# Optimization experiments

Measured on AMD Instinct MI355X. Metric: run time of the kernel, lower is better.

Reference implementation:

```python
import jax, jax.numpy as jnp
import numpy as np

DEPTH, DIM, HEADS, MLP, P, IMG, C = 6, 512, 8, 2048, 16, 224, 3
NPATCH = (IMG // P) ** 2  # 196
EPS = 1e-5


def setup_inputs() -> dict:
    key = jax.random.key(0)
    ks = jax.random.split(key, 16)
    s = 0.02
    return {
        "img": jax.random.normal(ks[0], (64, C, IMG, IMG), jnp.float32),
        "patch_w": jax.random.normal(ks[1], (DIM, C * P * P), jnp.float32) * s,
        "patch_b": jax.random.normal(ks[2], (DIM,), jnp.float32) * s,
        "cls_token": jax.random.normal(ks[3], (1, 1, DIM), jnp.float32),
        "pos_emb": jax.random.normal(ks[4], (1, NPATCH + 1, DIM), jnp.float32),
        "in_proj_w": jax.random.normal(ks[5], (DEPTH, 3 * DIM, DIM), jnp.float32) * s,
        "in_proj_b": jax.random.normal(ks[6], (DEPTH, 3 * DIM), jnp.float32) * s,
        "out_proj_w": jax.random.normal(ks[7], (DEPTH, DIM, DIM), jnp.float32) * s,
        "out_proj_b": jax.random.normal(ks[8], (DEPTH, DIM), jnp.float32) * s,
        "ln1_w": jnp.ones((DEPTH, DIM), jnp.float32),
        "ln1_b": jnp.zeros((DEPTH, DIM), jnp.float32),
        "fc1_w": jax.random.normal(ks[9], (DEPTH, MLP, DIM), jnp.float32) * s,
        "fc1_b": jax.random.normal(ks[10], (DEPTH, MLP), jnp.float32) * s,
        "fc2_w": jax.random.normal(ks[11], (DEPTH, DIM, MLP), jnp.float32) * s,
        "fc2_b": jax.random.normal(ks[12], (DEPTH, DIM), jnp.float32) * s,
        "ln2_w": jnp.ones((DEPTH, DIM), jnp.float32),
        "ln2_b": jnp.zeros((DEPTH, DIM), jnp.float32),
    }


def _ln(x, w, b):
    m = jnp.mean(x, -1, keepdims=True)
    v = jnp.mean(jnp.square(x - m), -1, keepdims=True)
    return (x - m) * jax.lax.rsqrt(v + EPS) * w + b


def _patchify(img):
    # b c (h p1) (w p2) -> b (h w) (p1 p2 c), lucidrains ViT ordering
    B = img.shape[0]
    g = IMG // P
    x = img.reshape(B, C, g, P, g, P)
    x = x.transpose(0, 2, 4, 3, 5, 1)  # B, h, w, p1, p2, c
    return x.reshape(B, g * g, P * P * C)


def _vit(img, patch_w, patch_b, cls_token, pos_emb, in_proj_w, in_proj_b,
         out_proj_w, out_proj_b, ln1_w, ln1_b, fc1_w, fc1_b, fc2_w, fc2_b,
         ln2_w, ln2_b):
    B = img.shape[0]
    hd = DIM // HEADS
    x = _patchify(img) @ patch_w.T + patch_b          # [B, 196, 512]
    cls = jnp.broadcast_to(cls_token, (B, 1, DIM))
    x = jnp.concatenate([cls, x], axis=1) + pos_emb   # [B, 197, 512]
    N = x.shape[1]
    for i in range(DEPTH):
        res = x
        qkv = x @ in_proj_w[i].T + in_proj_b[i]       # [B, N, 3*512]
        q, k, v = jnp.split(qkv, 3, axis=-1)
        q = q.reshape(B, N, HEADS, hd).transpose(0, 2, 1, 3)
        k = k.reshape(B, N, HEADS, hd).transpose(0, 2, 1, 3)
        v = v.reshape(B, N, HEADS, hd).transpose(0, 2, 1, 3)
        scores = jnp.einsum('bhnd,bhmd->bhnm', q, k) / jnp.sqrt(jnp.float32(hd))
        probs = jax.nn.softmax(scores, axis=-1)
        ctx = jnp.einsum('bhnm,bhmd->bhnd', probs, v)
        ctx = ctx.transpose(0, 2, 1, 3).reshape(B, N, DIM)
        x = ctx @ out_proj_w[i].T + out_proj_b[i] + res
        x = _ln(x, ln1_w[i], ln1_b[i])
        res = x
        h = jax.nn.gelu(x @ fc1_w[i].T + fc1_b[i], approximate=False)
        x = h @ fc2_w[i].T + fc2_b[i] + res
        x = _ln(x, ln2_w[i], ln2_b[i])
    return x[:, 0]  # ToCLS_Slice: forward returns CLS token [B, 512]


def reference(img, patch_w, patch_b, cls_token, pos_emb, in_proj_w, in_proj_b,
              out_proj_w, out_proj_b, ln1_w, ln1_b, fc1_w, fc1_b, fc2_w, fc2_b,
              ln2_w, ln2_b):
    return _vit(img, patch_w, patch_b, cls_token, pos_emb, in_proj_w, in_proj_b,
                out_proj_w, out_proj_b, ln1_w, ln1_b, fc1_w, fc1_b, fc2_w, fc2_b,
                ln2_w, ln2_b)
```

## Files before the change

### kernel.cpp

```cpp
#include <hip/hip_runtime.h>
#include <hip/hip_bf16.h>

typedef __hip_bfloat16 hb;
typedef __bf16 bf16x8 __attribute__((ext_vector_type(8)));
typedef float f32x4 __attribute__((ext_vector_type(4)));

#define N_DEPTH 6
#define N_DIM   512
#define N_HEADS 8
#define N_MLP   2048
#define N_TOK   197
#define N_PATCH 196
#define N_BATCH 64
#define ROWS    (N_BATCH * N_TOK)
#define ROWS_PAD 12672
#define PROWS   (N_BATCH * N_PATCH)

#define OFF_WPATCH 0u
#define OFF_WQKV   786432u
#define OFF_WOUT   10223616u
#define OFF_WFC1   13369344u
#define OFF_WFC2   25952256u
#define OFF_XBF    38535168u
#define OFF_CTX    51511296u
#define OFF_BIG    64487424u
#define OFF_XF     116391936u
#define OFF_H1     142344192u

__device__ __forceinline__ void gl2lds(const hb* g, hb* l) {
    __builtin_amdgcn_global_load_lds((const __attribute__((address_space(1))) unsigned int*)g,
                                     (__attribute__((address_space(3))) unsigned int*)l, 16, 0, 0);
}


__global__ void cvt_bf16_kernel(const float* __restrict__ in, hb* __restrict__ out, int n) {
    int t = blockIdx.x * 256 + threadIdx.x;
    if (t < n) out[t] = __float2bfloat16(in[t]);
}

__global__ void patchify_kernel(const float* __restrict__ img, hb* __restrict__ Xp) {
    int t = blockIdx.x * 256 + threadIdx.x;
    if (t >= PROWS * 768) return;
    int r = t / 768, j = t % 768;
    int b = r / 196, p = r % 196;
    int ph = p / 14, pw = p % 14;
    int p1 = j / 48, jr = j % 48;
    int p2 = jr / 3, c = jr % 3;
    float v = img[(((size_t)b * 3 + c) * 224 + ph * 16 + p1) * 224 + pw * 16 + p2];
    Xp[t] = __float2bfloat16(v);
}

__global__ void cls_init_kernel(const float* __restrict__ cls, const float* __restrict__ pos,
                                float* __restrict__ xf, hb* __restrict__ xb) {
    int t = blockIdx.x * 256 + threadIdx.x;
    int b = t >> 9, c = t & 511;
    float v = cls[c] + pos[c];
    size_t off = ((size_t)b * N_TOK) * N_DIM + c;
    xf[off] = v;
    xb[off] = __float2bfloat16(v);
}

__global__ void zero_pads_kernel(float* __restrict__ xf, hb* __restrict__ xb, hb* __restrict__ ctx) {
    int t = blockIdx.x * 256 + threadIdx.x;
    size_t off = (size_t)ROWS * N_DIM + t;
    xf[off] = 0.f;
    xb[off] = __float2bfloat16(0.f);
    ctx[off] = __float2bfloat16(0.f);
}

__global__ void extract_cls_kernel(const float* __restrict__ xf, float* __restrict__ out) {
    int t = blockIdx.x * 256 + threadIdx.x;
    int b = t >> 9, c = t & 511;
    out[t] = xf[((size_t)b * N_TOK) * N_DIM + c];
}


__global__ void __launch_bounds__(256) ln_kernel(const float* __restrict__ in,
                                                 const float* __restrict__ w, const float* __restrict__ b,
                                                 float* __restrict__ outf, hb* __restrict__ outb, int rows) {
    int row = blockIdx.x * 4 + (threadIdx.x >> 6);
    int lane = threadIdx.x & 63;
    if (row >= rows) return;
    const float* p = in + (size_t)row * N_DIM;
    float4 v0 = *(const float4*)(p + lane * 8);
    float4 v1 = *(const float4*)(p + lane * 8 + 4);
    float xs[8] = {v0.x, v0.y, v0.z, v0.w, v1.x, v1.y, v1.z, v1.w};
    float s = 0.f, q = 0.f;
#pragma unroll
    for (int j = 0; j < 8; ++j) { s += xs[j]; q += xs[j] * xs[j]; }
#pragma unroll
    for (int o = 32; o > 0; o >>= 1) { s += __shfl_xor(s, o); q += __shfl_xor(q, o); }
    float mean = s * (1.f / 512.f);
    float var = q * (1.f / 512.f) - mean * mean;
    float r = rsqrtf(var + 1e-5f);
    float4 w0 = *(const float4*)(w + lane * 8);
    float4 w1 = *(const float4*)(w + lane * 8 + 4);
    float4 b0 = *(const float4*)(b + lane * 8);
    float4 b1 = *(const float4*)(b + lane * 8 + 4);
    float ws8[8] = {w0.x, w0.y, w0.z, w0.w, w1.x, w1.y, w1.z, w1.w};
    float bs8[8] = {b0.x, b0.y, b0.z, b0.w, b1.x, b1.y, b1.z, b1.w};
    float of[8] __attribute__((aligned(16)));
    hb tb[8] __attribute__((aligned(16)));
#pragma unroll
    for (int j = 0; j < 8; ++j) {
        float y = (xs[j] - mean) * r * ws8[j] + bs8[j];
        of[j] = y;
        tb[j] = __float2bfloat16(y);
    }
    *(float4*)(outf + (size_t)row * N_DIM + lane * 8)     = *(const float4*)&of[0];
    *(float4*)(outf + (size_t)row * N_DIM + lane * 8 + 4) = *(const float4*)&of[4];
    *(float4*)(outb + (size_t)row * N_DIM + lane * 8)     = *(const float4*)&tb[0];
}


template <int MODE>
__global__ void __launch_bounds__(256) gemm_bt(const hb* __restrict__ A, const hb* __restrict__ B,
                                               const float* __restrict__ bias, int K, int N,
                                               hb* __restrict__ outb, float* __restrict__ outf,
                                               const float* __restrict__ res, const float* __restrict__ pos) {
    __shared__ hb Sm[8192];
    hb* As = Sm;
    hb* Bs = Sm + 4096;
    const int tid = threadIdx.x;
    const int lane = tid & 63, wid = tid >> 6;
    const int wr = wid >> 1, wc = wid & 1;
    const int quad = lane >> 4, r16 = lane & 15;
    const int m0 = blockIdx.y * 128, n0 = blockIdx.x * 128;

    const int r0 = lane >> 2;
    const int c0 = (lane & 3) ^ ((lane >> 3) & 3);
    const hb* ga0 = A + (size_t)(m0 + wid * 32 + r0) * K + c0 * 8;
    const hb* ga1 = ga0 + (size_t)16 * K;
    const hb* gb0 = B + (size_t)(n0 + wid * 32 + r0) * K + c0 * 8;
    const hb* gb1 = gb0 + (size_t)16 * K;
    hb* la0 = As + (wid * 32) * 32;
    hb* la1 = la0 + 16 * 32;
    hb* lb0 = Bs + (wid * 32) * 32;
    hb* lb1 = lb0 + 16 * 32;

    const int sw = (r16 >> 1) & 3;
    const int pa = (quad ^ sw) * 8;

    f32x4 acc[4][4] = {};

    for (int k0 = 0; k0 < K; k0 += 32) {
        gl2lds(ga0, la0);
        gl2lds(ga1, la1);
        gl2lds(gb0, lb0);
        gl2lds(gb1, lb1);
        ga0 += 32; ga1 += 32; gb0 += 32; gb1 += 32;
        __syncthreads();
        bf16x8 af[4], bfr[4];
#pragma unroll
        for (int t = 0; t < 4; ++t) {
            af[t]  = *(const bf16x8*)&As[(wr * 64 + t * 16 + r16) * 32 + pa];
            bfr[t] = *(const bf16x8*)&Bs[(wc * 64 + t * 16 + r16) * 32 + pa];
        }
#pragma unroll
        for (int mi = 0; mi < 4; ++mi)
#pragma unroll
            for (int nj = 0; nj < 4; ++nj)
                acc[mi][nj] = __builtin_amdgcn_mfma_f32_16x16x32_bf16(af[mi], bfr[nj], acc[mi][nj], 0, 0, 0);
        __syncthreads();
    }

    if constexpr (MODE == 0 || MODE == 1) {
        hb* Cb = Sm + wid * 2048;
#pragma unroll
        for (int p = 0; p < 2; ++p) {
#pragma unroll
            for (int nj2 = 0; nj2 < 2; ++nj2) {
                int nj = p * 2 + nj2;
                float bv = bias[n0 + wc * 64 + nj * 16 + r16];
#pragma unroll
                for (int mi = 0; mi < 4; ++mi)
#pragma unroll
                    for (int e = 0; e < 4; ++e) {
                        float v = acc[mi][nj][e] + bv;
                        if constexpr (MODE == 1) {
                            float y = 0.79788456f * (v + 0.044715f * v * v * v);
                            float t = 1.f - 2.f / (__expf(2.f * y) + 1.f);
                            v = 0.5f * v * (1.f + t);
                        }
                        Cb[(mi * 16 + quad * 4 + e) * 32 + nj2 * 16 + r16] = __float2bfloat16(v);
                    }
            }
#pragma unroll
            for (int it = 0; it < 4; ++it) {
                int idx = it * 64 + lane;
                int row = idx >> 2, ch = idx & 3;
                bf16x8 val = *(const bf16x8*)&Cb[row * 32 + ch * 8];
                *(bf16x8*)(outb + (size_t)(m0 + wr * 64 + row) * N + n0 + wc * 64 + p * 32 + ch * 8) = val;
            }
        }
    } else if constexpr (MODE == 2) {
#pragma unroll
        for (int nj = 0; nj < 4; ++nj) {
            int col = n0 + wc * 64 + nj * 16 + r16;
            float bv = bias[col];
#pragma unroll
            for (int mi = 0; mi < 4; ++mi)
#pragma unroll
                for (int e = 0; e < 4; ++e) {
                    int row = m0 + wr * 64 + mi * 16 + quad * 4 + e;
                    outf[(size_t)row * N + col] = acc[mi][nj][e] + bv + res[(size_t)row * N + col];
                }
        }
    } else {
#pragma unroll
        for (int nj = 0; nj < 4; ++nj) {
            int col = n0 + wc * 64 + nj * 16 + r16;
            float bv = bias[col];
#pragma unroll
            for (int mi = 0; mi < 4; ++mi)
#pragma unroll
                for (int e = 0; e < 4; ++e) {
                    int row = m0 + wr * 64 + mi * 16 + quad * 4 + e;
                    float v = acc[mi][nj][e] + bv;
                    int pidx = row % 196;
                    int row2 = row + row / 196 + 1;
                    v += pos[(size_t)(pidx + 1) * N_DIM + col];
                    outf[(size_t)row2 * N_DIM + col] = v;
                    outb[(size_t)row2 * N_DIM + col] = __float2bfloat16(v);
                }
        }
    }
}


__global__ void __launch_bounds__(256, 2) attn_kernel(const hb* __restrict__ qkv,
                                                      hb* __restrict__ ctx) {
    __shared__ hb Ks[224 * 64];
    __shared__ hb Vs[224 * 64];
    __shared__ hb Pb[4][16 * 40];
    const int bh = blockIdx.x;
    const int b = bh >> 3, h = bh & 7;
    const int tid = threadIdx.x, lane = tid & 63, wid = tid >> 6;
    const int quad = lane >> 4, r16 = lane & 15;
    const hb* base = qkv + (size_t)(b * N_TOK) * 1536 + h * 64;

#pragma unroll
    for (int i = 0; i < 7; ++i) {
        int idx = tid + i * 256;
        int m = idx >> 3, c = idx & 7;
        bf16x8 kv = {}, vv = {};
        if (m < 197) {
            kv = *(const bf16x8*)(base + (size_t)m * 1536 + 512 + c * 8);
            vv = *(const bf16x8*)(base + (size_t)m * 1536 + 1024 + c * 8);
        }
        *(bf16x8*)&Ks[m * 64 + c * 8] = kv;
        *(bf16x8*)&Vs[m * 64 + c * 8] = vv;
    }

    bf16x8 af[4][2];
#pragma unroll
    for (int mi = 0; mi < 4; ++mi) {
        int q = wid * 64 + mi * 16 + r16;
#pragma unroll
        for (int kc = 0; kc < 2; ++kc)
            af[mi][kc] = *(const bf16x8*)(base + (size_t)q * 1536 + kc * 32 + quad * 8);
    }

    f32x4 o[4][4] = {};
    float mst[4][4], lp[4][4];
#pragma unroll
    for (int mi = 0; mi < 4; ++mi)
#pragma unroll
        for (int e = 0; e < 4; ++e) { mst[mi][e] = -3.0e38f; lp[mi][e] = 0.f; }

    __syncthreads();

    const __bf16* VsB = (const __bf16*)Vs;
    for (int kt = 0; kt < 7; ++kt) {
        bf16x8 bk[2][2], bv[4];
#pragma unroll
        for (int nj = 0; nj < 2; ++nj)
#pragma unroll
            for (int kc = 0; kc < 2; ++kc)
                bk[nj][kc] = *(const bf16x8*)&Ks[(kt * 32 + nj * 16 + r16) * 64 + kc * 32 + quad * 8];
#pragma unroll
        for (int jd = 0; jd < 4; ++jd) {
            bf16x8 t;
#pragma unroll
            for (int j = 0; j < 8; ++j)
                t[j] = VsB[(kt * 32 + quad * 8 + j) * 64 + jd * 16 + r16];
            bv[jd] = t;
        }

        const bool v0 = (kt * 32 + r16) < N_TOK;
        const bool v1 = (kt * 32 + 16 + r16) < N_TOK;

#pragma unroll
        for (int mi = 0; mi < 4; ++mi) {
            f32x4 z = {};
            f32x4 s0v = __builtin_amdgcn_mfma_f32_16x16x32_bf16(af[mi][0], bk[0][0], z, 0, 0, 0);
            s0v = __builtin_amdgcn_mfma_f32_16x16x32_bf16(af[mi][1], bk[0][1], s0v, 0, 0, 0);
            f32x4 s1v = __builtin_amdgcn_mfma_f32_16x16x32_bf16(af[mi][0], bk[1][0], z, 0, 0, 0);
            s1v = __builtin_amdgcn_mfma_f32_16x16x32_bf16(af[mi][1], bk[1][1], s1v, 0, 0, 0);

            float al[4];
#pragma unroll
            for (int e = 0; e < 4; ++e) {
                float s0 = v0 ? s0v[e] * 0.125f : -1e30f;
                float s1 = v1 ? s1v[e] * 0.125f : -1e30f;
                float mx = fmaxf(s0, s1);
#pragma unroll
                for (int off = 1; off < 16; off <<= 1) mx = fmaxf(mx, __shfl_xor(mx, off));
                float mnew = fmaxf(mst[mi][e], mx);
                float alpha = __expf(mst[mi][e] - mnew);
                mst[mi][e] = mnew;
                float p0 = __expf(s0 - mnew);
                float p1 = __expf(s1 - mnew);
                lp[mi][e] = lp[mi][e] * alpha + p0 + p1;
                al[e] = alpha;
                int prow = (quad * 4 + e) * 40;
                Pb[wid][prow + r16]      = __float2bfloat16(p0);
                Pb[wid][prow + 16 + r16] = __float2bfloat16(p1);
            }
#pragma unroll
            for (int jd = 0; jd < 4; ++jd)
#pragma unroll
                for (int e = 0; e < 4; ++e) o[mi][jd][e] *= al[e];
            bf16x8 ap = *(const bf16x8*)&Pb[wid][r16 * 40 + quad * 8];
#pragma unroll
            for (int jd = 0; jd < 4; ++jd)
                o[mi][jd] = __builtin_amdgcn_mfma_f32_16x16x32_bf16(ap, bv[jd], o[mi][jd], 0, 0, 0);
        }
    }

#pragma unroll
    for (int mi = 0; mi < 4; ++mi) {
        float rl[4];
#pragma unroll
        for (int e = 0; e < 4; ++e) {
            float l = lp[mi][e];
#pragma unroll
            for (int off = 1; off < 16; off <<= 1) l += __shfl_xor(l, off);
            rl[e] = 1.f / l;
        }
        int qrow = wid * 64 + mi * 16 + quad * 4;
#pragma unroll
        for (int e = 0; e < 4; ++e) {
            int q = qrow + e;
            if (q < N_TOK) {
                hb* dst = ctx + ((size_t)(b * N_TOK + q)) * N_DIM + h * 64;
#pragma unroll
                for (int jd = 0; jd < 4; ++jd)
                    dst[jd * 16 + r16] = __float2bfloat16(o[mi][jd][e] * rl[e]);
            }
        }
    }
}


extern "C" void kernel_launch(void* const* d_in, const int* in_sizes, int n_in,
                              void* d_out, int out_size, void* d_ws, size_t ws_size,
                              hipStream_t stream) {
    (void)in_sizes; (void)n_in; (void)out_size; (void)ws_size;
    const float* img     = (const float*)d_in[0];
    const float* patch_w = (const float*)d_in[1];
    const float* patch_b = (const float*)d_in[2];
    const float* cls_t   = (const float*)d_in[3];
    const float* pos     = (const float*)d_in[4];
    const float* w_qkv   = (const float*)d_in[5];
    const float* b_qkv   = (const float*)d_in[6];
    const float* w_out   = (const float*)d_in[7];
    const float* b_out   = (const float*)d_in[8];
    const float* ln1w    = (const float*)d_in[9];
    const float* ln1b    = (const float*)d_in[10];
    const float* w_fc1   = (const float*)d_in[11];
    const float* b_fc1   = (const float*)d_in[12];
    const float* w_fc2   = (const float*)d_in[13];
    const float* b_fc2   = (const float*)d_in[14];
    const float* ln2w    = (const float*)d_in[15];
    const float* ln2b    = (const float*)d_in[16];

    char* ws = (char*)d_ws;
    hb* wPatch = (hb*)(ws + OFF_WPATCH);
    hb* wQKV   = (hb*)(ws + OFF_WQKV);
    hb* wOut   = (hb*)(ws + OFF_WOUT);
    hb* wFc1   = (hb*)(ws + OFF_WFC1);
    hb* wFc2   = (hb*)(ws + OFF_WFC2);
    hb* x_bf   = (hb*)(ws + OFF_XBF);
    hb* ctx    = (hb*)(ws + OFF_CTX);
    hb* Xp     = (hb*)(ws + OFF_BIG);
    hb* qkv    = (hb*)(ws + OFF_BIG);
    hb* hmid   = (hb*)(ws + OFF_BIG);
    float* x_f = (float*)(ws + OFF_XF);
    float* h1  = (float*)(ws + OFF_H1);

    auto cvt = [&](const float* src, hb* dst, int n) {
        cvt_bf16_kernel<<<dim3((n + 255) / 256), dim3(256), 0, stream>>>(src, dst, n);
    };
    cvt(patch_w, wPatch, 512 * 768);
    cvt(w_qkv, wQKV, N_DEPTH * 1536 * 512);
    cvt(w_out, wOut, N_DEPTH * 512 * 512);
    cvt(w_fc1, wFc1, N_DEPTH * 2048 * 512);
    cvt(w_fc2, wFc2, N_DEPTH * 512 * 2048);

    patchify_kernel<<<dim3((PROWS * 768 + 255) / 256), dim3(256), 0, stream>>>(img, Xp);
    gemm_bt<3><<<dim3(4, 98), dim3(256), 0, stream>>>(Xp, wPatch, patch_b, 768, 512,
                                                      x_bf, x_f, nullptr, pos);
    cls_init_kernel<<<dim3(128), dim3(256), 0, stream>>>(cls_t, pos, x_f, x_bf);
    zero_pads_kernel<<<dim3(128), dim3(256), 0, stream>>>(x_f, x_bf, ctx);

    for (int i = 0; i < N_DEPTH; ++i) {
        gemm_bt<0><<<dim3(12, 99), dim3(256), 0, stream>>>(x_bf, wQKV + (size_t)i * 1536 * 512,
                                                           b_qkv + i * 1536, 512, 1536,
                                                           qkv, nullptr, nullptr, nullptr);
        attn_kernel<<<dim3(512), dim3(256), 0, stream>>>(qkv, ctx);
        gemm_bt<2><<<dim3(4, 99), dim3(256), 0, stream>>>(ctx, wOut + (size_t)i * 512 * 512,
                                                          b_out + i * 512, 512, 512,
                                                          nullptr, h1, x_f, nullptr);
        ln_kernel<<<dim3(3152), dim3(256), 0, stream>>>(h1, ln1w + i * 512, ln1b + i * 512, x_f, x_bf, ROWS);
        gemm_bt<1><<<dim3(16, 99), dim3(256), 0, stream>>>(x_bf, wFc1 + (size_t)i * 2048 * 512,
                                                           b_fc1 + i * 2048, 512, 2048,
                                                           hmid, nullptr, nullptr, nullptr);
        gemm_bt<2><<<dim3(4, 99), dim3(256), 0, stream>>>(hmid, wFc2 + (size_t)i * 512 * 2048,
                                                          b_fc2 + i * 512, 2048, 512,
                                                          nullptr, h1, x_f, nullptr);
        ln_kernel<<<dim3(3152), dim3(256), 0, stream>>>(h1, ln2w + i * 512, ln2b + i * 512, x_f, x_bf, ROWS);
    }

    extract_cls_kernel<<<dim3(128), dim3(256), 0, stream>>>(x_f, (float*)d_out);
}
```

Baseline: 1.568 ms.

## Store GEMM operands in MFMA-fragment tiled layout and load fragments directly to registers

```diff
diff --git a/kernel.cpp b/kernel.cpp
--- a/kernel.cpp
+++ b/kernel.cpp
@@ -27,16 +27,36 @@
 #define OFF_XF     116391936u
 #define OFF_H1     142344192u
 
+__device__ __forceinline__ size_t swoff(int row, int k, int KB) {
+    return (size_t)((((row >> 7) * KB + (k >> 5)) * 2 + ((row >> 6) & 1)) * 4 + ((row >> 4) & 3)) * 512
+           + ((k >> 3) & 3) * 128 + (row & 15) * 8 + (k & 7);
+}
+
 __device__ __forceinline__ void gl2lds(const hb* g, hb* l) {
     __builtin_amdgcn_global_load_lds((const __attribute__((address_space(1))) unsigned int*)g,
                                      (__attribute__((address_space(3))) unsigned int*)l, 16, 0, 0);
 }
 
 
+__global__ void wsw_kernel(const float* __restrict__ W, hb* __restrict__ out, int K, int N) {
+    const int layer = blockIdx.y;
+    const float* Wl = W + (size_t)layer * N * K;
+    hb* ol = out + (size_t)layer * N * K;
+    int idx = blockIdx.x * 256 + threadIdx.x;
+    if (idx >= N * (K >> 3)) return;
+    int n = idx / (K >> 3), kc = idx % (K >> 3);
+    int k = kc * 8;
+    hb tmp[8] __attribute__((aligned(16)));
+#pragma unroll
+    for (int j = 0; j < 8; ++j) tmp[j] = __float2bfloat16(Wl[(size_t)n * K + k + j]);
+    *(float4*)(ol + swoff(n, k, K >> 5)) = *(const float4*)tmp;
+}
+
 __global__ void cvt_bf16_kernel(const float* __restrict__ in, hb* __restrict__ out, int n) {
     int t = blockIdx.x * 256 + threadIdx.x;
     if (t < n) out[t] = __float2bfloat16(in[t]);
 }
+
 
 __global__ void patchify_kernel(const float* __restrict__ img, hb* __restrict__ Xp) {
     int t = blockIdx.x * 256 + threadIdx.x;
@@ -55,17 +75,19 @@
     int t = blockIdx.x * 256 + threadIdx.x;
     int b = t >> 9, c = t & 511;
     float v = cls[c] + pos[c];
-    size_t off = ((size_t)b * N_TOK) * N_DIM + c;
-    xf[off] = v;
-    xb[off] = __float2bfloat16(v);
+    int row = b * N_TOK;
+    xf[(size_t)row * N_DIM + c] = v;
+    xb[swoff(row, c, 16)] = __float2bfloat16(v);
 }
 
 __global__ void zero_pads_kernel(float* __restrict__ xf, hb* __restrict__ xb, hb* __restrict__ ctx) {
     int t = blockIdx.x * 256 + threadIdx.x;
-    size_t off = (size_t)ROWS * N_DIM + t;
-    xf[off] = 0.f;
-    xb[off] = __float2bfloat16(0.f);
-    ctx[off] = __float2bfloat16(0.f);
+    xf[(size_t)ROWS * N_DIM + t] = 0.f;
+    int kb = t >> 11, r2 = t & 2047;
+    size_t off = (size_t)((98 * 16 + kb) * 2 + 1) * 2048 + r2;
+    hb z = __float2bfloat16(0.f);
+    xb[off] = z;
+    ctx[off] = z;
 }
 
 __global__ void extract_cls_kernel(const float* __restrict__ xf, float* __restrict__ out) {
@@ -109,15 +131,115 @@
     }
     *(float4*)(outf + (size_t)row * N_DIM + lane * 8)     = *(const float4*)&of[0];
     *(float4*)(outf + (size_t)row * N_DIM + lane * 8 + 4) = *(const float4*)&of[4];
-    *(float4*)(outb + (size_t)row * N_DIM + lane * 8)     = *(const float4*)&tb[0];
-}
-
-
-template <int MODE>
-__global__ void __launch_bounds__(256) gemm_bt(const hb* __restrict__ A, const hb* __restrict__ B,
+    *(float4*)(outb + swoff(row, lane * 8, 16)) = *(const float4*)tb;
+}
+
+
+template <int K, int MODE>
+__global__ void __launch_bounds__(256) gemm_sw(const hb* __restrict__ A, const hb* __restrict__ B,
+                                               const float* __restrict__ bias, int N,
+                                               hb* __restrict__ outb, float* __restrict__ outf,
+                                               const float* __restrict__ res) {
+    constexpr int KB = K / 32;
+    __shared__ hb Sm[4][2560];
+    const int tid = threadIdx.x;
+    const int lane = tid & 63, wid = tid >> 6;
+    const int wr = wid >> 1, wc = wid & 1;
+    const int quad = lane >> 4, r16 = lane & 15;
+    const int mb = blockIdx.y, nb = blockIdx.x;
+    const int m0 = mb * 128, n0 = nb * 128;
+
+    const hb* pa = A + (size_t)mb * KB * 4096 + wr * 2048 + lane * 8;
+    const hb* pb = B + (size_t)nb * KB * 4096 + wc * 2048 + lane * 8;
+
+    f32x4 acc[4][4] = {};
+    bf16x8 af[4], bfr[4];
+#pragma unroll
+    for (int t = 0; t < 4; ++t) {
+        af[t]  = *(const bf16x8*)(pa + t * 512);
+        bfr[t] = *(const bf16x8*)(pb + t * 512);
+    }
+#pragma unroll 2
+    for (int kb = 0; kb < KB; ++kb) {
+        bf16x8 an[4], bn[4];
+        if (kb + 1 < KB) {
+            size_t o = (size_t)(kb + 1) * 4096;
+#pragma unroll
+            for (int t = 0; t < 4; ++t) {
+                an[t] = *(const bf16x8*)(pa + o + t * 512);
+                bn[t] = *(const bf16x8*)(pb + o + t * 512);
+            }
+        }
+#pragma unroll
+        for (int mi = 0; mi < 4; ++mi)
+#pragma unroll
+            for (int nj = 0; nj < 4; ++nj)
+                acc[mi][nj] = __builtin_amdgcn_mfma_f32_16x16x32_bf16(af[mi], bfr[nj], acc[mi][nj], 0, 0, 0);
+        if (kb + 1 < KB) {
+#pragma unroll
+            for (int t = 0; t < 4; ++t) { af[t] = an[t]; bfr[t] = bn[t]; }
+        }
+    }
+
+    if constexpr (MODE == 0 || MODE == 1) {
+        hb* Cb = &Sm[wid][0];
+#pragma unroll
+        for (int p = 0; p < 2; ++p) {
+#pragma unroll
+            for (int nj2 = 0; nj2 < 2; ++nj2) {
+                int nj = p * 2 + nj2;
+                float bv = bias[n0 + wc * 64 + nj * 16 + r16];
+#pragma unroll
+                for (int mi = 0; mi < 4; ++mi)
+#pragma unroll
+                    for (int e = 0; e < 4; ++e) {
+                        float v = acc[mi][nj][e] + bv;
+                        if constexpr (MODE == 1) {
+                            float y = 0.79788456f * (v + 0.044715f * v * v * v);
+                            float t = 1.f - 2.f / (__expf(2.f * y) + 1.f);
+                            v = 0.5f * v * (1.f + t);
+                        }
+                        Cb[(mi * 16 + quad * 4 + e) * 40 + nj2 * 16 + r16] = __float2bfloat16(v);
+                    }
+            }
+            if constexpr (MODE == 0) {
+#pragma unroll
+                for (int it = 0; it < 4; ++it) {
+                    int idx = it * 64 + lane;
+                    int row = idx >> 2, ch = idx & 3;
+                    bf16x8 val = *(const bf16x8*)&Cb[row * 40 + ch * 8];
+                    *(bf16x8*)(outb + (size_t)(m0 + wr * 64 + row) * N + n0 + wc * 64 + p * 32 + ch * 8) = val;
+                }
+            } else {
+                size_t base = ((((size_t)mb * (N >> 5) + ((n0 + wc * 64 + p * 32) >> 5)) * 2 + wr) * 4) * 512;
+#pragma unroll
+                for (int it = 0; it < 4; ++it) {
+                    bf16x8 val = *(const bf16x8*)&Cb[(it * 16 + r16) * 40 + quad * 8];
+                    *(bf16x8*)(outb + base + it * 512 + lane * 8) = val;
+                }
+            }
+        }
+    } else {
+#pragma unroll
+        for (int nj = 0; nj < 4; ++nj) {
+            int col = n0 + wc * 64 + nj * 16 + r16;
+            float bv = bias[col];
+#pragma unroll
+            for (int mi = 0; mi < 4; ++mi)
+#pragma unroll
+                for (int e = 0; e < 4; ++e) {
+                    int row = m0 + wr * 64 + mi * 16 + quad * 4 + e;
+                    outf[(size_t)row * N + col] = acc[mi][nj][e] + bv + res[(size_t)row * N + col];
+                }
+        }
+    }
+}
+
+
+__global__ void __launch_bounds__(256) gemm_pe(const hb* __restrict__ A, const hb* __restrict__ B,
                                                const float* __restrict__ bias, int K, int N,
                                                hb* __restrict__ outb, float* __restrict__ outf,
-                                               const float* __restrict__ res, const float* __restrict__ pos) {
+                                               const float* __restrict__ pos) {
     __shared__ hb Sm[8192];
     hb* As = Sm;
     hb* Bs = Sm + 4096;
@@ -137,12 +259,10 @@
     hb* la1 = la0 + 16 * 32;
     hb* lb0 = Bs + (wid * 32) * 32;
     hb* lb1 = lb0 + 16 * 32;
-
     const int sw = (r16 >> 1) & 3;
     const int pa = (quad ^ sw) * 8;
 
     f32x4 acc[4][4] = {};
-
     for (int k0 = 0; k0 < K; k0 += 32) {
         gl2lds(ga0, la0);
         gl2lds(ga1, la1);
@@ -164,66 +284,22 @@
         __syncthreads();
     }
 
-    if constexpr (MODE == 0 || MODE == 1) {
-        hb* Cb = Sm + wid * 2048;
-#pragma unroll
-        for (int p = 0; p < 2; ++p) {
-#pragma unroll
-            for (int nj2 = 0; nj2 < 2; ++nj2) {
-                int nj = p * 2 + nj2;
-                float bv = bias[n0 + wc * 64 + nj * 16 + r16];
-#pragma unroll
-                for (int mi = 0; mi < 4; ++mi)
-#pragma unroll
-                    for (int e = 0; e < 4; ++e) {
-                        float v = acc[mi][nj][e] + bv;
-                        if constexpr (MODE == 1) {
-                            float y = 0.79788456f * (v + 0.044715f * v * v * v);
-                            float t = 1.f - 2.f / (__expf(2.f * y) + 1.f);
-                            v = 0.5f * v * (1.f + t);
-                        }
-                        Cb[(mi * 16 + quad * 4 + e) * 32 + nj2 * 16 + r16] = __float2bfloat16(v);
-                    }
-            }
-#pragma unroll
-            for (int it = 0; it < 4; ++it) {
-                int idx = it * 64 + lane;
-                int row = idx >> 2, ch = idx & 3;
-                bf16x8 val = *(const bf16x8*)&Cb[row * 32 + ch * 8];
-                *(bf16x8*)(outb + (size_t)(m0 + wr * 64 + row) * N + n0 + wc * 64 + p * 32 + ch * 8) = val;
-            }
-        }
-    } else if constexpr (MODE == 2) {
-#pragma unroll
-        for (int nj = 0; nj < 4; ++nj) {
-            int col = n0 + wc * 64 + nj * 16 + r16;
-            float bv = bias[col];
-#pragma unroll
-            for (int mi = 0; mi < 4; ++mi)
-#pragma unroll
-                for (int e = 0; e < 4; ++e) {
-                    int row = m0 + wr * 64 + mi * 16 + quad * 4 + e;
-                    outf[(size_t)row * N + col] = acc[mi][nj][e] + bv + res[(size_t)row * N + col];
-                }
-        }
-    } else {
-#pragma unroll
-        for (int nj = 0; nj < 4; ++nj) {
-            int col = n0 + wc * 64 + nj * 16 + r16;
-            float bv = bias[col];
-#pragma unroll
-            for (int mi = 0; mi < 4; ++mi)
-#pragma unroll
-                for (int e = 0; e < 4; ++e) {
-                    int row = m0 + wr * 64 + mi * 16 + quad * 4 + e;
-                    float v = acc[mi][nj][e] + bv;
-                    int pidx = row % 196;
-                    int row2 = row + row / 196 + 1;
-                    v += pos[(size_t)(pidx + 1) * N_DIM + col];
-                    outf[(size_t)row2 * N_DIM + col] = v;
-                    outb[(size_t)row2 * N_DIM + col] = __float2bfloat16(v);
-                }
-        }
+#pragma unroll
+    for (int nj = 0; nj < 4; ++nj) {
+        int col = n0 + wc * 64 + nj * 16 + r16;
+        float bv = bias[col];
+#pragma unroll
+        for (int mi = 0; mi < 4; ++mi)
+#pragma unroll
+            for (int e = 0; e < 4; ++e) {
+                int row = m0 + wr * 64 + mi * 16 + quad * 4 + e;
+                float v = acc[mi][nj][e] + bv;
+                int pidx = row % 196;
+                int row2 = row + row / 196 + 1;
+                v += pos[(size_t)(pidx + 1) * N_DIM + col];
+                outf[(size_t)row2 * N_DIM + col] = v;
+                outb[swoff(row2, col, 16)] = __float2bfloat16(v);
+            }
     }
 }
 
@@ -343,10 +419,10 @@
         for (int e = 0; e < 4; ++e) {
             int q = qrow + e;
             if (q < N_TOK) {
-                hb* dst = ctx + ((size_t)(b * N_TOK + q)) * N_DIM + h * 64;
+                int row = b * N_TOK + q;
 #pragma unroll
                 for (int jd = 0; jd < 4; ++jd)
-                    dst[jd * 16 + r16] = __float2bfloat16(o[mi][jd][e] * rl[e]);
+                    ctx[swoff(row, h * 64 + jd * 16 + r16, 16)] = __float2bfloat16(o[mi][jd][e] * rl[e]);
             }
         }
     }
@@ -389,36 +465,28 @@
     float* x_f = (float*)(ws + OFF_XF);
     float* h1  = (float*)(ws + OFF_H1);
 
-    auto cvt = [&](const float* src, hb* dst, int n) {
-        cvt_bf16_kernel<<<dim3((n + 255) / 256), dim3(256), 0, stream>>>(src, dst, n);
-    };
-    cvt(patch_w, wPatch, 512 * 768);
-    cvt(w_qkv, wQKV, N_DEPTH * 1536 * 512);
-    cvt(w_out, wOut, N_DEPTH * 512 * 512);
-    cvt(w_fc1, wFc1, N_DEPTH * 2048 * 512);
-    cvt(w_fc2, wFc2, N_DEPTH * 512 * 2048);
+    cvt_bf16_kernel<<<dim3((512 * 768 + 255) / 256), dim3(256), 0, stream>>>(patch_w, wPatch, 512 * 768);
+    wsw_kernel<<<dim3(384, 6), dim3(256), 0, stream>>>(w_qkv, wQKV, 512, 1536);
+    wsw_kernel<<<dim3(128, 6), dim3(256), 0, stream>>>(w_out, wOut, 512, 512);
+    wsw_kernel<<<dim3(512, 6), dim3(256), 0, stream>>>(w_fc1, wFc1, 512, 2048);
+    wsw_kernel<<<dim3(512, 6), dim3(256), 0, stream>>>(w_fc2, wFc2, 2048, 512);
 
     patchify_kernel<<<dim3((PROWS * 768 + 255) / 256), dim3(256), 0, stream>>>(img, Xp);
-    gemm_bt<3><<<dim3(4, 98), dim3(256), 0, stream>>>(Xp, wPatch, patch_b, 768, 512,
-                                                      x_bf, x_f, nullptr, pos);
+    gemm_pe<<<dim3(4, 98), dim3(256), 0, stream>>>(Xp, wPatch, patch_b, 768, 512, x_bf, x_f, pos);
     cls_init_kernel<<<dim3(128), dim3(256), 0, stream>>>(cls_t, pos, x_f, x_bf);
     zero_pads_kernel<<<dim3(128), dim3(256), 0, stream>>>(x_f, x_bf, ctx);
 
     for (int i = 0; i < N_DEPTH; ++i) {
-        gemm_bt<0><<<dim3(12, 99), dim3(256), 0, stream>>>(x_bf, wQKV + (size_t)i * 1536 * 512,
-                                                           b_qkv + i * 1536, 512, 1536,
-                                                           qkv, nullptr, nullptr, nullptr);
+        gemm_sw<512, 0><<<dim3(12, 99), dim3(256), 0, stream>>>(x_bf, wQKV + (size_t)i * 1536 * 512,
+                                                                b_qkv + i * 1536, 1536, qkv, nullptr, nullptr);
         attn_kernel<<<dim3(512), dim3(256), 0, stream>>>(qkv, ctx);
-        gemm_bt<2><<<dim3(4, 99), dim3(256), 0, stream>>>(ctx, wOut + (size_t)i * 512 * 512,
-                                                          b_out + i * 512, 512, 512,
-                                                          nullptr, h1, x_f, nullptr);
+        gemm_sw<512, 2><<<dim3(4, 99), dim3(256), 0, stream>>>(ctx, wOut + (size_t)i * 512 * 512,
+                                                               b_out + i * 512, 512, nullptr, h1, x_f);
         ln_kernel<<<dim3(3152), dim3(256), 0, stream>>>(h1, ln1w + i * 512, ln1b + i * 512, x_f, x_bf, ROWS);
-        gemm_bt<1><<<dim3(16, 99), dim3(256), 0, stream>>>(x_bf, wFc1 + (size_t)i * 2048 * 512,
-                                                           b_fc1 + i * 2048, 512, 2048,
-                                                           hmid, nullptr, nullptr, nullptr);
-        gemm_bt<2><<<dim3(4, 99), dim3(256), 0, stream>>>(hmid, wFc2 + (size_t)i * 512 * 2048,
-                                                          b_fc2 + i * 512, 2048, 512,
-                                                          nullptr, h1, x_f, nullptr);
+        gemm_sw<512, 1><<<dim3(16, 99), dim3(256), 0, stream>>>(x_bf, wFc1 + (size_t)i * 2048 * 512,
+                                                                b_fc1 + i * 2048, 2048, hmid, nullptr, nullptr);
+        gemm_sw<2048, 2><<<dim3(4, 99), dim3(256), 0, stream>>>(hmid, wFc2 + (size_t)i * 512 * 2048,
+                                                                b_fc2 + i * 512, 512, nullptr, h1, x_f);
         ln_kernel<<<dim3(3152), dim3(256), 0, stream>>>(h1, ln2w + i * 512, ln2b + i * 512, x_f, x_bf, ROWS);
     }
 
```

Result: faster. 1.489 ms (-5.0%).
